# Kernel tuning notes

Measured on AMD Instinct MI355X. Metric: run time of the kernel, lower is better.

The kernel has to match this reference:

```python
import jax, jax.numpy as jnp
import numpy as np
from jax import lax
jax.config.update('jax_enable_x64', True)

SR = 44100
BLOCK = 512
N_MELS = 80
N_ALLPASS = 256
N_HARM = 512
N_NOISE = 256
HID = 256
B = 16
NF = 400
T = NF * BLOCK
N_OUT = N_ALLPASS + N_HARM + N_NOISE


def upsample(sig, factor):
    # torch: interpolate(cat(sig, sig[-1:]), size=n*factor+1, mode='linear', align_corners=True)[:-1]
    b, n, c = sig.shape
    ext = jnp.concatenate([sig, sig[:, -1:]], axis=1)  # (b, n+1, c)
    w = (jnp.arange(factor, dtype=jnp.float32) / factor)[None, None, :, None]
    up = ext[:, :-1, None, :] * (1.0 - w) + ext[:, 1:, None, :] * w
    return up.reshape(b, n * factor, c)


def hann_periodic(n):
    return 0.5 - 0.5 * jnp.cos(2.0 * np.pi * jnp.arange(n, dtype=jnp.float32) / n)


def freq_impulse_response(mag, hann_window, half_width=None):
    # mag: (b, nf, m) complex -> ir: (b, nf, 2*(m-1)) in causal (rolled) form
    ir = jnp.fft.irfft(mag).astype(jnp.float32)
    n = ir.shape[-1]
    if hann_window:
        if half_width is None:
            w = jnp.roll(hann_periodic(n), n // 2)
            ir = jnp.roll(ir * w, n // 2, axis=-1)
        else:
            # dynamic hann window with per-frame half width (b, nf, 1)
            w = jnp.arange(-(n // 2), (n + 1) // 2, dtype=jnp.float32) / half_width
            w = jnp.where(w > 1.0, 0.0, w)
            w = (1.0 + jnp.cos(np.pi * w)) * 0.5
            ir = jnp.roll(ir, n // 2, axis=-1) * w
    else:
        ir = jnp.roll(ir, n // 2, axis=-1)
    return ir


def fft_convolve(audio, ir):
    b, t = audio.shape
    nf, ir_size = ir.shape[1], ir.shape[2]
    hop = t // nf
    frame = 2 * hop
    fft_size = frame + ir_size - 1
    chunks = jnp.pad(audio, ((0, 0), (hop, hop))).reshape(b, nf + 2, hop)
    frames = jnp.concatenate([chunks[:, :-1], chunks[:, 1:]], axis=-1)  # (b, nf+1, frame)
    bart = 1.0 - jnp.abs(2.0 * jnp.arange(frame, dtype=jnp.float32) / frame - 1.0)
    frames = frames * bart
    ir_ext = jnp.concatenate([ir, ir[:, -1:]], axis=1)  # repeat last IR frame
    out_f = jnp.fft.irfft(jnp.fft.rfft(frames, fft_size) * jnp.fft.rfft(ir_ext, fft_size), fft_size).astype(jnp.float32)
    n_out = nf + 1
    length = (n_out - 1) * hop + fft_size
    idx = (jnp.arange(n_out)[:, None] * hop + jnp.arange(fft_size)[None, :]).reshape(-1)
    out = jnp.zeros((b, length), jnp.float32).at[:, idx].add(out_f.reshape(b, -1))
    return out[:, hop:t + hop]


def conv1d_same(x, w, bias):
    y = lax.conv_general_dilated(x, w, (1,), [(1, 1)], dimension_numbers=('NCH', 'OIH', 'NCH'))
    return y + bias[None, :, None]


def mel2ctrl(mel, phase, conv1_w, conv1_b, gn_g, gn_b, conv2_w, conv2_b, phase_w, phase_b, ln_g, ln_b, out_w, out_b):
    h = conv1d_same(mel.transpose(0, 2, 1), conv1_w, conv1_b)  # (b, 256, nf)
    b, c, l = h.shape
    g = h.reshape(b, 4, c // 4, l)  # GroupNorm(4, 256)
    mu = g.mean((2, 3), keepdims=True)
    var = g.var((2, 3), keepdims=True)
    h = ((g - mu) / jnp.sqrt(var + 1e-5)).reshape(b, c, l)
    h = h * gn_g[None, :, None] + gn_b[None, :, None]
    h = jnp.where(h >= 0, h, 0.01 * h)  # LeakyReLU
    h = conv1d_same(h, conv2_w, conv2_b).transpose(0, 2, 1)  # (b, nf, 256)
    pe = jnp.concatenate([jnp.sin(phase), jnp.cos(phase)], axis=-1) @ phase_w.T + phase_b
    h = h + pe
    mu = h.mean(-1, keepdims=True)
    var = h.var(-1, keepdims=True)
    h = (h - mu) / jnp.sqrt(var + 1e-5) * ln_g + ln_b
    out = h @ out_w.T + out_b
    gd = out[..., :N_ALLPASS]
    hm = out[..., N_ALLPASS:N_ALLPASS + N_HARM]
    nm = out[..., N_ALLPASS + N_HARM:]
    return gd, hm, nm


def setup_inputs():
    key = jax.random.key(0)
    ks = jax.random.split(key, 8)
    s = 0.02
    return {
        'mel_frames': jax.random.normal(ks[0], (B, NF, N_MELS), jnp.float32),
        'f0_frames': jax.random.uniform(ks[1], (B, NF, 1), jnp.float32) * 400.0 + 100.0,
        'initial_phase': jnp.zeros((B, 1, 1), jnp.float32),
        'uniform_noise': jax.random.uniform(ks[2], (B, T), jnp.float32),
        'conv1_w': jax.random.normal(ks[3], (HID, N_MELS, 3), jnp.float32) * s,
        'conv1_b': jnp.zeros((HID,), jnp.float32),
        'gn_g': jnp.ones((HID,), jnp.float32),
        'gn_b': jnp.zeros((HID,), jnp.float32),
        'conv2_w': jax.random.normal(ks[4], (HID, HID, 3), jnp.float32) * s,
        'conv2_b': jnp.zeros((HID,), jnp.float32),
        'phase_w': jax.random.normal(ks[5], (HID, 2), jnp.float32) * s,
        'phase_b': jnp.zeros((HID,), jnp.float32),
        'ln_g': jnp.ones((HID,), jnp.float32),
        'ln_b': jnp.zeros((HID,), jnp.float32),
        'out_w': jax.random.normal(ks[6], (N_OUT, HID), jnp.float32) * s,
        'out_b': jnp.zeros((N_OUT,), jnp.float32),
    }


def reference(mel_frames, f0_frames, initial_phase, uniform_noise, conv1_w, conv1_b, gn_g, gn_b, conv2_w, conv2_b, phase_w, phase_b, ln_g, ln_b, out_w, out_b):
    f0 = upsample(f0_frames, BLOCK)  # (B, T, 1)
    # double-precision wrapped phase accumulation
    x = jnp.cumsum(f0.astype(jnp.float64) / SR, axis=1) + initial_phase.astype(jnp.float64) / (2.0 * np.pi)
    x = (x - jnp.round(x)).astype(jnp.float32)
    phase_frames = 2.0 * np.pi * x[:, ::BLOCK, :]  # (B, NF, 1)
    gd_raw, hm_raw, nm_raw = mel2ctrl(mel_frames, phase_frames, conv1_w, conv1_b, gn_g, gn_b, conv2_w, conv2_b, phase_w, phase_b, ln_g, ln_b, out_w, out_b)
    group_delay = np.pi * jnp.tanh(gd_raw)
    src_param = jnp.exp(hm_raw)
    noise_param = jnp.exp(nm_raw) / 128.0
    combtooth = jnp.sinc(SR * x / (f0 + 0.001))[..., 0]  # (B, T)
    allpass = jnp.exp(1j * jnp.cumsum(group_delay, axis=-1).astype(jnp.complex64))
    harmonic = fft_convolve(combtooth, freq_impulse_response(allpass, hann_window=False))
    half_width = 1.5 * SR / (f0_frames + 0.001)  # (B, NF, 1)
    harmonic = fft_convolve(harmonic, freq_impulse_response(src_param.astype(jnp.complex64), True, half_width))
    noise = uniform_noise * 2.0 - 1.0
    noise = fft_convolve(noise, freq_impulse_response(noise_param.astype(jnp.complex64), True, None))
    signal = harmonic + noise
    return signal, phase_frames, harmonic, noise
```

## Files before the change

kernel.cpp:

```cpp
#include <hip/hip_runtime.h>
#include <math.h>

#define BATCH 16
#define NF_ 400
#define TLEN 204800
#define NMELS 80
#define HID 256
#define SRD 44100.0

static constexpr size_t S_   = 1638400;
static constexpr size_t FRSZ = (size_t)6416 * 1028;
static constexpr size_t OFF_A    = 0;
static constexpr size_t OFF_JN   = FRSZ;
static constexpr size_t OFF_SSP  = 2 * FRSZ;
static constexpr size_t OFF_IR1  = OFF_SSP + 2 * S_;
static constexpr size_t OFF_IR3  = OFF_IR1 + 3264000;
static constexpr size_t OFF_FSUM = OFF_IR3 + 3264000;
static constexpr size_t OFF_PREF = OFF_FSUM + 12800;
static constexpr size_t OFF_GN   = OFF_PREF + 12800;

__device__ __forceinline__ float cs8_f0_at(const float* f0f, int b, int n, int k) {
    float a = f0f[b * NF_ + n];
    float c = f0f[b * NF_ + min(n + 1, NF_ - 1)];
    float w = (float)k * (1.0f / 512.0f);
    return __fadd_rn(__fmul_rn(a, 1.0f - w), __fmul_rn(c, w));
}

__global__ void cs8_fsum(const float* __restrict__ f0f, double* __restrict__ fsum) {
    int gid = blockIdx.x * blockDim.x + threadIdx.x;
    if (gid >= BATCH * NF_) return;
    int b = gid / NF_, n = gid % NF_;
    double s = 0.0;
    for (int k = 0; k < 512; ++k) s += (double)cs8_f0_at(f0f, b, n, k) / SRD;
    fsum[gid] = s;
}

__global__ void cs8_prefix(const double* __restrict__ fsum, double* __restrict__ pref) {
    int b = threadIdx.x;
    if (b >= BATCH) return;
    double run = 0.0;
    for (int n = 0; n < NF_; ++n) { pref[b * NF_ + n] = run; run += fsum[b * NF_ + n]; }
}

__global__ __launch_bounds__(512) void cs8_phase(const float* __restrict__ f0f,
        const float* __restrict__ ip, const double* __restrict__ pref,
        float* __restrict__ frA, float* __restrict__ phase_out) {
    __shared__ double sc[512];
    int b = blockIdx.x / NF_, n = blockIdx.x % NF_;
    int k = threadIdx.x;
    float f0 = cs8_f0_at(f0f, b, n, k);
    sc[k] = (double)f0 / SRD;
    __syncthreads();
    for (int off = 1; off < 512; off <<= 1) {
        double v = (k >= off) ? sc[k - off] : 0.0;
        __syncthreads();
        sc[k] += v;
        __syncthreads();
    }
    double xd = pref[b * NF_ + n] + sc[k] + (double)ip[b] / (2.0 * M_PI);
    xd -= rint(xd);
    float xf = (float)xd;
    double zd = 44100.0 * (double)xf / ((double)f0 + 0.001);
    double pz = M_PI * zd;
    float cv = (zd == 0.0) ? 1.0f : (float)(sin(pz) / pz);
    float wb = (float)k * (1.0f / 512.0f);
    size_t row = (size_t)(b * 401 + n) * 1028;
    frA[row + 512 + k]  = cv * (1.0f - wb);
    frA[row + 1028 + k] = cv * wb;
    if (k == 0) phase_out[b * NF_ + n] = (float)(2.0 * M_PI * (double)xf);
}

__global__ __launch_bounds__(256) void cs8_conv1x3(const float* __restrict__ mel,
        const float* __restrict__ w1, const float* __restrict__ b1, float* __restrict__ h1) {
    __shared__ float m3[3][NMELS];
    int b = blockIdx.x / NF_, l = blockIdx.x % NF_;
    int tid = threadIdx.x;
    for (int i = tid; i < 3 * NMELS; i += 256) {
        int tap = i / NMELS, ic = i % NMELS;
        int li = l + tap - 1;
        m3[tap][ic] = (li >= 0 && li < NF_) ? mel[((size_t)b * NF_ + li) * NMELS + ic] : 0.0f;
    }
    __syncthreads();
    int oc = tid;
    double acc = (double)b1[oc];
    const float* wp = w1 + (size_t)oc * NMELS * 3;
    for (int ic = 0; ic < NMELS; ++ic)
        acc += (double)m3[0][ic] * (double)wp[ic * 3]
             + (double)m3[1][ic] * (double)wp[ic * 3 + 1]
             + (double)m3[2][ic] * (double)wp[ic * 3 + 2];
    h1[((size_t)b * NF_ + l) * HID + oc] = (float)acc;
}

__global__ __launch_bounds__(256) void cs8_gnstats(const float* __restrict__ h1, float* __restrict__ gn) {
    __shared__ double rs[256], rq[256];
    int b = blockIdx.x >> 2, g = blockIdx.x & 3;
    int tid = threadIdx.x;
    double s = 0.0, q = 0.0;
    for (int i = tid; i < 64 * NF_; i += 256) {
        int l = i >> 6, c = g * 64 + (i & 63);
        float v = h1[((size_t)b * NF_ + l) * HID + c];
        s += v; q += (double)v * v;
    }
    rs[tid] = s; rq[tid] = q;
    __syncthreads();
    for (int off = 128; off > 0; off >>= 1) {
        if (tid < off) { rs[tid] += rs[tid + off]; rq[tid] += rq[tid + off]; }
        __syncthreads();
    }
    if (tid == 0) {
        double mu = rs[0] / (64.0 * NF_);
        double var = rq[0] / (64.0 * NF_) - mu * mu;
        gn[blockIdx.x * 2] = (float)mu;
        gn[blockIdx.x * 2 + 1] = (float)(1.0 / sqrt(var + 1e-5));
    }
}

__global__ __launch_bounds__(256) void cs8_conv2ln(const float* __restrict__ h1,
        const float* __restrict__ gn, const float* __restrict__ gng, const float* __restrict__ gnb,
        const float* __restrict__ w2, const float* __restrict__ b2,
        const float* __restrict__ pw, const float* __restrict__ pb,
        const float* __restrict__ lng, const float* __restrict__ lnb,
        const float* __restrict__ phase, float* __restrict__ h2) {
    __shared__ float cols[10][HID];
    __shared__ double rsum[256], rsq[256];
    int b = blockIdx.x / 50, l0 = (blockIdx.x % 50) * 8;
    int tid = threadIdx.x;
    for (int i = tid; i < 10 * HID; i += 256) {
        int lc = i >> 8, c = i & 255;
        int l = l0 + lc - 1;
        float v = 0.0f;
        if (l >= 0 && l < NF_) {
            float hv = h1[((size_t)b * NF_ + l) * HID + c];
            int g = c >> 6;
            double vv = ((double)hv - (double)gn[(b * 4 + g) * 2]) * (double)gn[(b * 4 + g) * 2 + 1]
                        * (double)gng[c] + (double)gnb[c];
            v = (float)(vv >= 0.0 ? vv : 0.01 * vv);
        }
        cols[lc][c] = v;
    }
    __syncthreads();
    int oc = tid;
    double acc[8];
    #pragma unroll
    for (int lt = 0; lt < 8; ++lt) acc[lt] = (double)b2[oc];
    const float* wp = w2 + (size_t)oc * HID * 3;
    for (int ic = 0; ic < HID; ++ic) {
        double w0 = (double)wp[ic * 3], w1v = (double)wp[ic * 3 + 1], w2v = (double)wp[ic * 3 + 2];
        float cc[10];
        #pragma unroll
        for (int j = 0; j < 10; ++j) cc[j] = cols[j][ic];
        #pragma unroll
        for (int lt = 0; lt < 8; ++lt)
            acc[lt] += (double)cc[lt] * w0 + (double)cc[lt + 1] * w1v + (double)cc[lt + 2] * w2v;
    }
    for (int lt = 0; lt < 8; ++lt) {
        int l = l0 + lt;
        double ph = (double)phase[b * NF_ + l];
        double sp, cp; sincos(ph, &sp, &cp);
        double v = acc[lt] + sp * (double)pw[oc * 2] + cp * (double)pw[oc * 2 + 1] + (double)pb[oc];
        rsum[tid] = v; rsq[tid] = v * v;
        __syncthreads();
        for (int off = 128; off > 0; off >>= 1) {
            if (tid < off) { rsum[tid] += rsum[tid + off]; rsq[tid] += rsq[tid + off]; }
            __syncthreads();
        }
        double mu = rsum[0] * (1.0 / 256.0);
        double var = rsq[0] * (1.0 / 256.0) - mu * mu;
        double rstd = 1.0 / sqrt(var + 1e-5);
        __syncthreads();
        h2[((size_t)b * NF_ + l) * HID + oc] = (float)((v - mu) * rstd * (double)lng[oc] + (double)lnb[oc]);
    }
}

__global__ __launch_bounds__(256) void cs8_proj(const float* __restrict__ h2,
        const float* __restrict__ ow, const float* __restrict__ ob,
        float* __restrict__ phi, float* __restrict__ srcspec, float* __restrict__ nspec) {
    __shared__ float hrow[8][HID];
    __shared__ double ssc[256];
    int b = blockIdx.x / 50, l0 = (blockIdx.x % 50) * 8;
    int tid = threadIdx.x;
    for (int i = tid; i < 8 * HID; i += 256) {
        int lc = i >> 8, c = i & 255;
        hrow[lc][c] = h2[((size_t)b * NF_ + l0 + lc) * HID + c];
    }
    __syncthreads();
    double a0[8], a1[8], a2[8], a3[8];
    #pragma unroll
    for (int lt = 0; lt < 8; ++lt) {
        a0[lt] = (double)ob[tid];       a1[lt] = (double)ob[256 + tid];
        a2[lt] = (double)ob[512 + tid]; a3[lt] = (double)ob[768 + tid];
    }
    const float* w0p = ow + (size_t)tid * HID;
    const float* w1p = ow + (size_t)(256 + tid) * HID;
    const float* w2p = ow + (size_t)(512 + tid) * HID;
    const float* w3p = ow + (size_t)(768 + tid) * HID;
    for (int ic = 0; ic < HID; ++ic) {
        double w0 = (double)w0p[ic], w1v = (double)w1p[ic], w2v = (double)w2p[ic], w3v = (double)w3p[ic];
        #pragma unroll
        for (int lt = 0; lt < 8; ++lt) {
            double h = (double)hrow[lt][ic];
            a0[lt] += h * w0; a1[lt] += h * w1v; a2[lt] += h * w2v; a3[lt] += h * w3v;
        }
    }
    for (int lt = 0; lt < 8; ++lt) {
        size_t bl = (size_t)b * NF_ + (l0 + lt);
        double gdv = M_PI * tanh(a0[lt]);
        ssc[tid] = gdv;
        __syncthreads();
        for (int off = 1; off < 256; off <<= 1) {
            double v = (tid >= off) ? ssc[tid - off] : 0.0;
            __syncthreads();
            ssc[tid] += v;
            __syncthreads();
        }
        phi[bl * 256 + tid] = (float)ssc[tid];
        __syncthreads();
        srcspec[bl * 512 + tid] = (float)exp(a1[lt]);
        srcspec[bl * 512 + 256 + tid] = (float)exp(a2[lt]);
        nspec[bl * 256 + tid] = (float)(exp(a3[lt]) * (1.0 / 128.0));
    }
}

__global__ __launch_bounds__(256) void cs8_ir_allpass(const float* __restrict__ phi, float* __restrict__ ir1) {
    __shared__ float cph[256], sph[256];
    size_t bl = blockIdx.x;
    int tid = threadIdx.x;
    {
        float ph = phi[bl * 256 + tid];
        cph[tid] = 2.0f * cosf(ph); sph[tid] = 2.0f * sinf(ph);
    }
    __syncthreads();
    for (int t = tid; t < 510; t += 256) {
        double ang = 2.0 * M_PI * (double)t / 510.0;
        double srd_, crd; sincos(ang, &srd_, &crd);
        double sj, cj;    sincos(16.0 * ang, &sj, &cj);
        float crf = (float)crd, srf = (float)srd_;
        double cD = crd, sD = srd_;
        float acc = 0.5f * (cph[0] + ((t & 1) ? -cph[255] : cph[255]));
        for (int k0 = 1; k0 <= 254; k0 += 16) {
            float c = (float)cD, s = (float)sD;
            int ke = min(k0 + 16, 255);
            for (int k = k0; k < ke; ++k) {
                acc += cph[k] * c - sph[k] * s;
                float cn = c * crf - s * srf;
                float sn = s * crf + c * srf;
                c = cn; s = sn;
            }
            double nc = cD * cj - sD * sj;
            double ns = sD * cj + cD * sj;
            cD = nc; sD = ns;
        }
        int j = t + 255; if (j >= 510) j -= 510;
        ir1[bl * 510 + j] = acc * (1.0f / 510.0f);
    }
}

__device__ __forceinline__ float cs8_hw_win(int j, float hw) {
    float wv = (float)(j - 511) / hw;
    if (wv > 1.0f) wv = 0.0f;
    return (1.0f + cosf((float)M_PI * wv)) * 0.5f;
}

__global__ __launch_bounds__(256) void cs8_ir_src(const float* __restrict__ srcspec,
        const float* __restrict__ f0f, float* __restrict__ ir2) {
    __shared__ float sp[512];
    size_t bl = blockIdx.x;
    int b = blockIdx.x / NF_, l = blockIdx.x % NF_;
    int tid = threadIdx.x;
    sp[tid] = 2.0f * srcspec[bl * 512 + tid];
    sp[tid + 256] = 2.0f * srcspec[bl * 512 + 256 + tid];
    __syncthreads();
    float hw = 66150.0f / (f0f[b * NF_ + l] + 0.001f);
    for (int t = tid; t < 512; t += 256) {
        double ang = 2.0 * M_PI * (double)t / 1022.0;
        double srd_, crd; sincos(ang, &srd_, &crd);
        double sj, cj;    sincos(16.0 * ang, &sj, &cj);
        float crf = (float)crd, srf = (float)srd_;
        double cD = crd, sD = srd_;
        float acc = 0.5f * (sp[0] + ((t & 1) ? -sp[511] : sp[511]));
        for (int k0 = 1; k0 <= 510; k0 += 16) {
            float c = (float)cD, s = (float)sD;
            int ke = min(k0 + 16, 511);
            for (int k = k0; k < ke; ++k) {
                acc += sp[k] * c;
                float cn = c * crf - s * srf;
                float sn = s * crf + c * srf;
                c = cn; s = sn;
            }
            double nc = cD * cj - sD * sj;
            double ns = sD * cj + cD * sj;
            cD = nc; sD = ns;
        }
        float raw = acc * (1.0f / 1022.0f);
        {
            int j = t + 511; if (j >= 1022) j -= 1022;
            ir2[bl * 1022 + j] = raw * cs8_hw_win(j, hw);
        }
        if (t >= 1 && t <= 510) {
            int j = 511 - t;
            ir2[bl * 1022 + j] = raw * cs8_hw_win(j, hw);
        }
    }
}

__global__ __launch_bounds__(256) void cs8_ir_noise(const float* __restrict__ nspec, float* __restrict__ ir3) {
    __shared__ float sp[256];
    size_t bl = blockIdx.x;
    int t = threadIdx.x;
    sp[t] = 2.0f * nspec[bl * 256 + t];
    __syncthreads();
    double ang = 2.0 * M_PI * (double)t / 510.0;
    double srd_, crd; sincos(ang, &srd_, &crd);
    double sj, cj;    sincos(16.0 * ang, &sj, &cj);
    float crf = (float)crd, srf = (float)srd_;
    double cD = crd, sD = srd_;
    float acc = 0.5f * (sp[0] + ((t & 1) ? -sp[255] : sp[255]));
    for (int k0 = 1; k0 <= 254; k0 += 16) {
        float c = (float)cD, s = (float)sD;
        int ke = min(k0 + 16, 255);
        for (int k = k0; k < ke; ++k) {
            acc += sp[k] * c;
            float cn = c * crf - s * srf;
            float sn = s * crf + c * srf;
            c = cn; s = sn;
        }
        double nc = cD * cj - sD * sj;
        double ns = sD * cj + cD * sj;
        cD = nc; sD = ns;
    }
    float raw = acc * (1.0f / 510.0f);
    {
        int j = t + 255; if (j >= 510) j -= 510;
        float win = 0.5f - 0.5f * cosf((float)(2.0 * M_PI) * (float)j / 510.0f);
        ir3[bl * 510 + j] = raw * win;
    }
    if (t >= 1 && t <= 254) {
        int j = 255 - t;
        float win = 0.5f - 0.5f * cosf((float)(2.0 * M_PI) * (float)j / 510.0f);
        ir3[bl * 510 + j] = raw * win;
    }
}

__global__ __launch_bounds__(256) void cs8_stagef(const float* __restrict__ audio,
        float* __restrict__ frw, float scale, float shift) {
    int bm = blockIdx.x;
    int b = bm / 401, m = bm % 401;
    int tid = threadIdx.x;
    for (int kk = tid; kk < 1028; kk += 256) {
        float v = 0.0f;
        if (kk < 1024) {
            int idx = (m << 9) + kk - 512;
            if (idx >= 0 && idx < TLEN) {
                float a = audio[(size_t)b * TLEN + idx] * scale + shift;
                float bart = 1.0f - fabsf((float)kk * (1.0f / 512.0f) - 1.0f);
                v = a * bart;
            }
        }
        frw[(size_t)bm * 1028 + kk] = v;
    }
}

__device__ __forceinline__ int cs8_swz(int B) { return B ^ ((B >> 3) & 7); }

__device__ __forceinline__ void cs8_fma8(const float4 F, const float4 A,
        const float4 B, const float4 C, float acc[8]) {
    const float w[12] = {A.x,A.y,A.z,A.w,B.x,B.y,B.z,B.w,C.x,C.y,C.z,C.w};
    #pragma unroll
    for (int a = 0; a < 8; ++a)
        acc[a] += F.x * w[8 - a] + F.y * w[9 - a] + F.z * w[10 - a] + F.w * w[11 - a];
}

template<int IRS, int NFRM, int MOFF, int FOUT>
__global__ __launch_bounds__(256) void cs8_conv(const float* __restrict__ frw,
        const float* __restrict__ ir, float* __restrict__ out) {
    constexpr int PAD = 515;
    constexpr int R = IRS - 1 + PAD;
    constexpr int W = (R + 526) & ~3;
    __shared__ __align__(16) float sir[NFRM][W];
    int b = blockIdx.x / 100, q = blockIdx.x % 100;
    int t0 = q * 2048;
    int m_lo = (t0 >> 9) + MOFF;
    int tid = threadIdx.x;

    for (int i = tid; i < NFRM * W; i += 256) {
        int fi = i / W, x = i - fi * W;
        int j = R - x;
        int m = m_lo + fi;
        float v = 0.0f;
        if (j >= 0 && j < IRS && m >= 0 && m <= 400)
            v = ir[((size_t)b * NF_ + min(m, 399)) * IRS + j];
        int p = (cs8_swz(x >> 2) << 2) | (x & 3);
        sir[fi][p] = v;
    }
    __syncthreads();

    int tb = t0 + tid * 8;
    int wt0 = tid & ~63;
    float acc[8] = {0, 0, 0, 0, 0, 0, 0, 0};
    #pragma unroll
    for (int fi = 0; fi < NFRM; ++fi) {
        int m = m_lo + fi;
        if (m < 0 || m > 400) continue;
        int d0w = t0 + wt0 * 8 + 512 - (m << 9);
        int klo = max(0, d0w - (IRS - 1));
        int khi = min(1023, d0w + 511);
        if (klo > khi) continue;
        int kcs = __builtin_amdgcn_readfirstlane(klo & ~3);
        int nch = ((__builtin_amdgcn_readfirstlane(khi) - kcs) >> 2) + 1;
        int d0 = t0 + tid * 8 + 512 - (m << 9);
        int Bb = (R - d0 + kcs - 8) >> 2;
        const float4* row4 = (const float4*)&sir[fi][0];
        const float4* fp4 = (const float4*)(frw + (size_t)(b * 401 + m) * 1028 + kcs);
        float4 r0 = row4[cs8_swz(Bb)];
        float4 r1 = row4[cs8_swz(Bb + 1)];
        float4 r2;
        int c = 0;
        for (; c + 3 <= nch; c += 3) {
            float4 F0 = fp4[c];
            r2 = row4[cs8_swz(Bb + c + 2)];
            cs8_fma8(F0, r0, r1, r2, acc);
            float4 F1 = fp4[c + 1];
            r0 = row4[cs8_swz(Bb + c + 3)];
            cs8_fma8(F1, r1, r2, r0, acc);
            float4 F2 = fp4[c + 2];
            r1 = row4[cs8_swz(Bb + c + 4)];
            cs8_fma8(F2, r2, r0, r1, acc);
        }
        for (; c < nch; ++c) {
            float4 F = fp4[c];
            r2 = row4[cs8_swz(Bb + c + 2)];
            cs8_fma8(F, r0, r1, r2, acc);
            r0 = r1; r1 = r2;
        }
    }
    if (FOUT == 0) {
        float* o = out + (size_t)b * TLEN + tb;
        *(float4*)o = make_float4(acc[0], acc[1], acc[2], acc[3]);
        *(float4*)(o + 4) = make_float4(acc[4], acc[5], acc[6], acc[7]);
    } else {
        int km = tb & 511;
        int m1 = tb >> 9;
        float* r1p = out + (size_t)(b * 401 + m1) * 1028;
        float bw[8];
        #pragma unroll
        for (int j2 = 0; j2 < 8; ++j2) bw[j2] = (float)(km + j2) * (1.0f / 512.0f);
        *(float4*)(r1p + 512 + km) = make_float4(acc[0] * (1.f - bw[0]), acc[1] * (1.f - bw[1]),
                                                 acc[2] * (1.f - bw[2]), acc[3] * (1.f - bw[3]));
        *(float4*)(r1p + 512 + km + 4) = make_float4(acc[4] * (1.f - bw[4]), acc[5] * (1.f - bw[5]),
                                                     acc[6] * (1.f - bw[6]), acc[7] * (1.f - bw[7]));
        float* r2p = r1p + 1028;
        *(float4*)(r2p + km) = make_float4(acc[0] * bw[0], acc[1] * bw[1], acc[2] * bw[2], acc[3] * bw[3]);
        *(float4*)(r2p + km + 4) = make_float4(acc[4] * bw[4], acc[5] * bw[5], acc[6] * bw[6], acc[7] * bw[7]);
    }
}

__global__ void cs8_add(const float* __restrict__ a, const float* __restrict__ b,
                        float* __restrict__ o, int n4) {
    int i = blockIdx.x * blockDim.x + threadIdx.x;
    if (i < n4) {
        float4 x = ((const float4*)a)[i];
        float4 y = ((const float4*)b)[i];
        ((float4*)o)[i] = make_float4(x.x + y.x, x.y + y.y, x.z + y.z, x.w + y.w);
    }
}

extern "C" void kernel_launch(void* const* d_in, const int* in_sizes, int n_in,
                              void* d_out, int out_size, void* d_ws, size_t ws_size,
                              hipStream_t stream) {
    const float* mel   = (const float*)d_in[0];
    const float* f0f   = (const float*)d_in[1];
    const float* ip    = (const float*)d_in[2];
    const float* unoi  = (const float*)d_in[3];
    const float* w1    = (const float*)d_in[4];
    const float* b1    = (const float*)d_in[5];
    const float* gng   = (const float*)d_in[6];
    const float* gnb   = (const float*)d_in[7];
    const float* w2    = (const float*)d_in[8];
    const float* b2    = (const float*)d_in[9];
    const float* pw    = (const float*)d_in[10];
    const float* pb    = (const float*)d_in[11];
    const float* lng   = (const float*)d_in[12];
    const float* lnb   = (const float*)d_in[13];
    const float* ow    = (const float*)d_in[14];
    const float* ob    = (const float*)d_in[15];
    float* out = (float*)d_out;
    float* ws  = (float*)d_ws;

    float*  frA  = ws + OFF_A;
    float*  frJ  = ws + OFF_JN;
    float*  h1   = ws + OFF_JN;
    float*  h2   = ws + OFF_JN + S_;
    float*  phi  = ws + OFF_JN + 2 * S_;
    float*  nsp  = ws + OFF_JN + 3 * S_;
    float*  ssp  = ws + OFF_SSP;
    float*  ir1  = ws + OFF_IR1;
    float*  ir3  = ws + OFF_IR3;
    float*  ir2  = ws + OFF_A;
    double* fsum = (double*)(ws + OFF_FSUM);
    double* pref = (double*)(ws + OFF_PREF);
    float*  gn   = ws + OFF_GN;

    float* out_sig   = out;
    float* out_phase = out + (size_t)BATCH * TLEN;
    float* out_harm  = out_phase + BATCH * NF_;
    float* out_noise = out_harm + (size_t)BATCH * TLEN;

    hipMemsetAsync(frA, 0, FRSZ * sizeof(float), stream);
    cs8_fsum<<<25, 256, 0, stream>>>(f0f, fsum);
    cs8_prefix<<<1, 16, 0, stream>>>(fsum, pref);
    cs8_phase<<<BATCH * NF_, 512, 0, stream>>>(f0f, ip, pref, frA, out_phase);
    cs8_conv1x3<<<BATCH * NF_, 256, 0, stream>>>(mel, w1, b1, h1);
    cs8_gnstats<<<64, 256, 0, stream>>>(h1, gn);
    cs8_conv2ln<<<BATCH * 50, 256, 0, stream>>>(h1, gn, gng, gnb, w2, b2, pw, pb, lng, lnb, out_phase, h2);
    cs8_proj<<<BATCH * 50, 256, 0, stream>>>(h2, ow, ob, phi, ssp, nsp);
    cs8_ir_allpass<<<BATCH * NF_, 256, 0, stream>>>(phi, ir1);
    cs8_ir_noise<<<BATCH * NF_, 256, 0, stream>>>(nsp, ir3);
    cs8_stagef<<<BATCH * 401, 256, 0, stream>>>(unoi, frJ, 2.0f, -1.0f);
    cs8_conv<510, 6, -1, 0><<<BATCH * 100, 256, 0, stream>>>(frJ, ir3, out_noise);
    hipMemsetAsync(frJ, 0, FRSZ * sizeof(float), stream);
    cs8_conv<510, 6, -1, 1><<<BATCH * 100, 256, 0, stream>>>(frA, ir1, frJ);
    cs8_ir_src<<<BATCH * NF_, 256, 0, stream>>>(ssp, f0f, ir2);
    cs8_conv<1022, 7, -2, 0><<<BATCH * 100, 256, 0, stream>>>(frJ, ir2, out_harm);
    cs8_add<<<(BATCH * TLEN / 4 + 255) / 256, 256, 0, stream>>>(out_harm, out_noise, out_sig, BATCH * TLEN / 4);
}
```

Baseline: 2.819 ms.

## Stage frames in LDS and halve output tile for long-IR convolution

```diff
diff --git a/kernel.cpp b/kernel.cpp
--- a/kernel.cpp
+++ b/kernel.cpp
@@ -19,36 +19,36 @@
 static constexpr size_t OFF_PREF = OFF_FSUM + 12800;
 static constexpr size_t OFF_GN   = OFF_PREF + 12800;
 
-__device__ __forceinline__ float cs8_f0_at(const float* f0f, int b, int n, int k) {
+__device__ __forceinline__ float cs9_f0_at(const float* f0f, int b, int n, int k) {
     float a = f0f[b * NF_ + n];
     float c = f0f[b * NF_ + min(n + 1, NF_ - 1)];
     float w = (float)k * (1.0f / 512.0f);
     return __fadd_rn(__fmul_rn(a, 1.0f - w), __fmul_rn(c, w));
 }
 
-__global__ void cs8_fsum(const float* __restrict__ f0f, double* __restrict__ fsum) {
+__global__ void cs9_fsum(const float* __restrict__ f0f, double* __restrict__ fsum) {
     int gid = blockIdx.x * blockDim.x + threadIdx.x;
     if (gid >= BATCH * NF_) return;
     int b = gid / NF_, n = gid % NF_;
     double s = 0.0;
-    for (int k = 0; k < 512; ++k) s += (double)cs8_f0_at(f0f, b, n, k) / SRD;
+    for (int k = 0; k < 512; ++k) s += (double)cs9_f0_at(f0f, b, n, k) / SRD;
     fsum[gid] = s;
 }
 
-__global__ void cs8_prefix(const double* __restrict__ fsum, double* __restrict__ pref) {
+__global__ void cs9_prefix(const double* __restrict__ fsum, double* __restrict__ pref) {
     int b = threadIdx.x;
     if (b >= BATCH) return;
     double run = 0.0;
     for (int n = 0; n < NF_; ++n) { pref[b * NF_ + n] = run; run += fsum[b * NF_ + n]; }
 }
 
-__global__ __launch_bounds__(512) void cs8_phase(const float* __restrict__ f0f,
+__global__ __launch_bounds__(512) void cs9_phase(const float* __restrict__ f0f,
         const float* __restrict__ ip, const double* __restrict__ pref,
         float* __restrict__ frA, float* __restrict__ phase_out) {
     __shared__ double sc[512];
     int b = blockIdx.x / NF_, n = blockIdx.x % NF_;
     int k = threadIdx.x;
-    float f0 = cs8_f0_at(f0f, b, n, k);
+    float f0 = cs9_f0_at(f0f, b, n, k);
     sc[k] = (double)f0 / SRD;
     __syncthreads();
     for (int off = 1; off < 512; off <<= 1) {
@@ -70,7 +70,7 @@
     if (k == 0) phase_out[b * NF_ + n] = (float)(2.0 * M_PI * (double)xf);
 }
 
-__global__ __launch_bounds__(256) void cs8_conv1x3(const float* __restrict__ mel,
+__global__ __launch_bounds__(256) void cs9_conv1x3(const float* __restrict__ mel,
         const float* __restrict__ w1, const float* __restrict__ b1, float* __restrict__ h1) {
     __shared__ float m3[3][NMELS];
     int b = blockIdx.x / NF_, l = blockIdx.x % NF_;
@@ -91,7 +91,7 @@
     h1[((size_t)b * NF_ + l) * HID + oc] = (float)acc;
 }
 
-__global__ __launch_bounds__(256) void cs8_gnstats(const float* __restrict__ h1, float* __restrict__ gn) {
+__global__ __launch_bounds__(256) void cs9_gnstats(const float* __restrict__ h1, float* __restrict__ gn) {
     __shared__ double rs[256], rq[256];
     int b = blockIdx.x >> 2, g = blockIdx.x & 3;
     int tid = threadIdx.x;
@@ -115,7 +115,7 @@
     }
 }
 
-__global__ __launch_bounds__(256) void cs8_conv2ln(const float* __restrict__ h1,
+__global__ __launch_bounds__(256) void cs9_conv2ln(const float* __restrict__ h1,
         const float* __restrict__ gn, const float* __restrict__ gng, const float* __restrict__ gnb,
         const float* __restrict__ w2, const float* __restrict__ b2,
         const float* __restrict__ pw, const float* __restrict__ pb,
@@ -172,7 +172,7 @@
     }
 }
 
-__global__ __launch_bounds__(256) void cs8_proj(const float* __restrict__ h2,
+__global__ __launch_bounds__(256) void cs9_proj(const float* __restrict__ h2,
         const float* __restrict__ ow, const float* __restrict__ ob,
         float* __restrict__ phi, float* __restrict__ srcspec, float* __restrict__ nspec) {
     __shared__ float hrow[8][HID];
@@ -221,7 +221,7 @@
     }
 }
 
-__global__ __launch_bounds__(256) void cs8_ir_allpass(const float* __restrict__ phi, float* __restrict__ ir1) {
+__global__ __launch_bounds__(256) void cs9_ir_allpass(const float* __restrict__ phi, float* __restrict__ ir1) {
     __shared__ float cph[256], sph[256];
     size_t bl = blockIdx.x;
     int tid = threadIdx.x;
@@ -255,13 +255,13 @@
     }
 }
 
-__device__ __forceinline__ float cs8_hw_win(int j, float hw) {
+__device__ __forceinline__ float cs9_hw_win(int j, float hw) {
     float wv = (float)(j - 511) / hw;
     if (wv > 1.0f) wv = 0.0f;
     return (1.0f + cosf((float)M_PI * wv)) * 0.5f;
 }
 
-__global__ __launch_bounds__(256) void cs8_ir_src(const float* __restrict__ srcspec,
+__global__ __launch_bounds__(256) void cs9_ir_src(const float* __restrict__ srcspec,
         const float* __restrict__ f0f, float* __restrict__ ir2) {
     __shared__ float sp[512];
     size_t bl = blockIdx.x;
@@ -294,16 +294,16 @@
         float raw = acc * (1.0f / 1022.0f);
         {
             int j = t + 511; if (j >= 1022) j -= 1022;
-            ir2[bl * 1022 + j] = raw * cs8_hw_win(j, hw);
+            ir2[bl * 1022 + j] = raw * cs9_hw_win(j, hw);
         }
         if (t >= 1 && t <= 510) {
             int j = 511 - t;
-            ir2[bl * 1022 + j] = raw * cs8_hw_win(j, hw);
-        }
-    }
-}
-
-__global__ __launch_bounds__(256) void cs8_ir_noise(const float* __restrict__ nspec, float* __restrict__ ir3) {
+            ir2[bl * 1022 + j] = raw * cs9_hw_win(j, hw);
+        }
+    }
+}
+
+__global__ __launch_bounds__(256) void cs9_ir_noise(const float* __restrict__ nspec, float* __restrict__ ir3) {
     __shared__ float sp[256];
     size_t bl = blockIdx.x;
     int t = threadIdx.x;
@@ -341,7 +341,7 @@
     }
 }
 
-__global__ __launch_bounds__(256) void cs8_stagef(const float* __restrict__ audio,
+__global__ __launch_bounds__(256) void cs9_stagef(const float* __restrict__ audio,
         float* __restrict__ frw, float scale, float shift) {
     int bm = blockIdx.x;
     int b = bm / 401, m = bm % 401;
@@ -360,25 +360,18 @@
     }
 }
 
-__device__ __forceinline__ int cs8_swz(int B) { return B ^ ((B >> 3) & 7); }
-
-__device__ __forceinline__ void cs8_fma8(const float4 F, const float4 A,
-        const float4 B, const float4 C, float acc[8]) {
-    const float w[12] = {A.x,A.y,A.z,A.w,B.x,B.y,B.z,B.w,C.x,C.y,C.z,C.w};
-    #pragma unroll
-    for (int a = 0; a < 8; ++a)
-        acc[a] += F.x * w[8 - a] + F.y * w[9 - a] + F.z * w[10 - a] + F.w * w[11 - a];
-}
-
-template<int IRS, int NFRM, int MOFF, int FOUT>
-__global__ __launch_bounds__(256) void cs8_conv(const float* __restrict__ frw,
+__device__ __forceinline__ int cs9_swz(int B) { return B ^ ((B >> 3) & 7); }
+
+template<int IRS, int NFRM, int MOFF, int OUTS, int FOUT>
+__global__ __launch_bounds__(256) void cs9_conv(const float* __restrict__ frw,
         const float* __restrict__ ir, float* __restrict__ out) {
-    constexpr int PAD = 515;
-    constexpr int R = IRS - 1 + PAD;
-    constexpr int W = (R + 526) & ~3;
+    constexpr int TILE = 256 * OUTS;
+    constexpr int R = IRS + (OUTS == 8 ? 514 : 266);
+    constexpr int W = (R + (OUTS == 8 ? 515 : 259) + 3) & ~3;
     __shared__ __align__(16) float sir[NFRM][W];
-    int b = blockIdx.x / 100, q = blockIdx.x % 100;
-    int t0 = q * 2048;
+    __shared__ __align__(16) float sfr[NFRM][1028];
+    int b = blockIdx.x / (TLEN / TILE), q = blockIdx.x % (TLEN / TILE);
+    int t0 = q * TILE;
     int m_lo = (t0 >> 9) + MOFF;
     int tid = threadIdx.x;
 
@@ -389,72 +382,147 @@
         float v = 0.0f;
         if (j >= 0 && j < IRS && m >= 0 && m <= 400)
             v = ir[((size_t)b * NF_ + min(m, 399)) * IRS + j];
-        int p = (cs8_swz(x >> 2) << 2) | (x & 3);
+        int p = (OUTS == 8) ? ((cs9_swz(x >> 2) << 2) | (x & 3)) : x;
         sir[fi][p] = v;
     }
-    __syncthreads();
-
-    int tb = t0 + tid * 8;
+    for (int i = tid; i < NFRM * 257; i += 256) {
+        int fi = i / 257, x4 = i - fi * 257;
+        int m = m_lo + fi;
+        float4 v = make_float4(0.f, 0.f, 0.f, 0.f);
+        if (m >= 0 && m <= 400)
+            v = ((const float4*)(frw + (size_t)(b * 401 + m) * 1028))[x4];
+        ((float4*)&sfr[fi][0])[x4] = v;
+    }
+    __syncthreads();
+
+    int tb = t0 + tid * OUTS;
     int wt0 = tid & ~63;
-    float acc[8] = {0, 0, 0, 0, 0, 0, 0, 0};
+    float acc[OUTS];
+    #pragma unroll
+    for (int a = 0; a < OUTS; ++a) acc[a] = 0.0f;
+
     #pragma unroll
     for (int fi = 0; fi < NFRM; ++fi) {
         int m = m_lo + fi;
         if (m < 0 || m > 400) continue;
-        int d0w = t0 + wt0 * 8 + 512 - (m << 9);
+        int d0w = __builtin_amdgcn_readfirstlane(t0 + wt0 * OUTS + 512 - (m << 9));
         int klo = max(0, d0w - (IRS - 1));
-        int khi = min(1023, d0w + 511);
+        int khi = min(1023, d0w + 64 * OUTS - 1);
         if (klo > khi) continue;
-        int kcs = __builtin_amdgcn_readfirstlane(klo & ~3);
-        int nch = ((__builtin_amdgcn_readfirstlane(khi) - kcs) >> 2) + 1;
-        int d0 = t0 + tid * 8 + 512 - (m << 9);
-        int Bb = (R - d0 + kcs - 8) >> 2;
+        int kcs = klo & ~3;
+        int nch = ((khi - kcs) >> 2) + 1;
+        int d0 = t0 + tid * OUTS + 512 - (m << 9);
         const float4* row4 = (const float4*)&sir[fi][0];
-        const float4* fp4 = (const float4*)(frw + (size_t)(b * 401 + m) * 1028 + kcs);
-        float4 r0 = row4[cs8_swz(Bb)];
-        float4 r1 = row4[cs8_swz(Bb + 1)];
-        float4 r2;
-        int c = 0;
-        for (; c + 3 <= nch; c += 3) {
-            float4 F0 = fp4[c];
-            r2 = row4[cs8_swz(Bb + c + 2)];
-            cs8_fma8(F0, r0, r1, r2, acc);
-            float4 F1 = fp4[c + 1];
-            r0 = row4[cs8_swz(Bb + c + 3)];
-            cs8_fma8(F1, r1, r2, r0, acc);
-            float4 F2 = fp4[c + 2];
-            r1 = row4[cs8_swz(Bb + c + 4)];
-            cs8_fma8(F2, r2, r0, r1, acc);
-        }
-        for (; c < nch; ++c) {
-            float4 F = fp4[c];
-            r2 = row4[cs8_swz(Bb + c + 2)];
-            cs8_fma8(F, r0, r1, r2, acc);
-            r0 = r1; r1 = r2;
-        }
-    }
+        const float4* fp4 = (const float4*)&sfr[fi][0] + (kcs >> 2);
+
+        if (OUTS == 4) {
+            int Bb = (R - d0 + kcs - 4) >> 2;
+            float4 A = row4[Bb];
+            int c = 0;
+            for (; c + 2 <= nch; c += 2) {
+                float4 Bv = row4[Bb + c + 1];
+                float4 F0 = fp4[c];
+                acc[0] += F0.x * Bv.x + F0.y * Bv.y + F0.z * Bv.z + F0.w * Bv.w;
+                acc[1] += F0.x * A.w  + F0.y * Bv.x + F0.z * Bv.y + F0.w * Bv.z;
+                acc[2] += F0.x * A.z  + F0.y * A.w  + F0.z * Bv.x + F0.w * Bv.y;
+                acc[3] += F0.x * A.y  + F0.y * A.z  + F0.z * A.w  + F0.w * Bv.x;
+                float4 A2 = row4[Bb + c + 2];
+                float4 F1 = fp4[c + 1];
+                acc[0] += F1.x * A2.x + F1.y * A2.y + F1.z * A2.z + F1.w * A2.w;
+                acc[1] += F1.x * Bv.w + F1.y * A2.x + F1.z * A2.y + F1.w * A2.z;
+                acc[2] += F1.x * Bv.z + F1.y * Bv.w + F1.z * A2.x + F1.w * A2.y;
+                acc[3] += F1.x * Bv.y + F1.y * Bv.z + F1.z * Bv.w + F1.w * A2.x;
+                A = A2;
+            }
+            for (; c < nch; ++c) {
+                float4 Bv = row4[Bb + c + 1];
+                float4 F0 = fp4[c];
+                acc[0] += F0.x * Bv.x + F0.y * Bv.y + F0.z * Bv.z + F0.w * Bv.w;
+                acc[1] += F0.x * A.w  + F0.y * Bv.x + F0.z * Bv.y + F0.w * Bv.z;
+                acc[2] += F0.x * A.z  + F0.y * A.w  + F0.z * Bv.x + F0.w * Bv.y;
+                acc[3] += F0.x * A.y  + F0.y * A.z  + F0.z * A.w  + F0.w * Bv.x;
+                A = Bv;
+            }
+        } else {
+            int Bb = (R - d0 + kcs - 8) >> 2;
+            float4 A = row4[cs9_swz(Bb)];
+            float4 Bv = row4[cs9_swz(Bb + 1)];
+            float4 C;
+            int c = 0;
+            for (; c + 3 <= nch; c += 3) {
+                float4 F0 = fp4[c];
+                C = row4[cs9_swz(Bb + c + 2)];
+                acc[0] += F0.x*C.x + F0.y*C.y + F0.z*C.z + F0.w*C.w;
+                acc[1] += F0.x*Bv.w + F0.y*C.x + F0.z*C.y + F0.w*C.z;
+                acc[2] += F0.x*Bv.z + F0.y*Bv.w + F0.z*C.x + F0.w*C.y;
+                acc[3] += F0.x*Bv.y + F0.y*Bv.z + F0.z*Bv.w + F0.w*C.x;
+                acc[4] += F0.x*Bv.x + F0.y*Bv.y + F0.z*Bv.z + F0.w*Bv.w;
+                acc[5] += F0.x*A.w + F0.y*Bv.x + F0.z*Bv.y + F0.w*Bv.z;
+                acc[6] += F0.x*A.z + F0.y*A.w + F0.z*Bv.x + F0.w*Bv.y;
+                acc[7] += F0.x*A.y + F0.y*A.z + F0.z*A.w + F0.w*Bv.x;
+                float4 F1 = fp4[c + 1];
+                A = row4[cs9_swz(Bb + c + 3)];
+                acc[0] += F1.x*A.x + F1.y*A.y + F1.z*A.z + F1.w*A.w;
+                acc[1] += F1.x*C.w + F1.y*A.x + F1.z*A.y + F1.w*A.z;
+                acc[2] += F1.x*C.z + F1.y*C.w + F1.z*A.x + F1.w*A.y;
+                acc[3] += F1.x*C.y + F1.y*C.z + F1.z*C.w + F1.w*A.x;
+                acc[4] += F1.x*C.x + F1.y*C.y + F1.z*C.z + F1.w*C.w;
+                acc[5] += F1.x*Bv.w + F1.y*C.x + F1.z*C.y + F1.w*C.z;
+                acc[6] += F1.x*Bv.z + F1.y*Bv.w + F1.z*C.x + F1.w*C.y;
+                acc[7] += F1.x*Bv.y + F1.y*Bv.z + F1.z*Bv.w + F1.w*C.x;
+                float4 F2 = fp4[c + 2];
+                Bv = row4[cs9_swz(Bb + c + 4)];
+                acc[0] += F2.x*Bv.x + F2.y*Bv.y + F2.z*Bv.z + F2.w*Bv.w;
+                acc[1] += F2.x*A.w + F2.y*Bv.x + F2.z*Bv.y + F2.w*Bv.z;
+                acc[2] += F2.x*A.z + F2.y*A.w + F2.z*Bv.x + F2.w*Bv.y;
+                acc[3] += F2.x*A.y + F2.y*A.z + F2.z*A.w + F2.w*Bv.x;
+                acc[4] += F2.x*A.x + F2.y*A.y + F2.z*A.z + F2.w*A.w;
+                acc[5] += F2.x*C.w + F2.y*A.x + F2.z*A.y + F2.w*A.z;
+                acc[6] += F2.x*C.z + F2.y*C.w + F2.z*A.x + F2.w*A.y;
+                acc[7] += F2.x*C.y + F2.y*C.z + F2.z*C.w + F2.w*A.x;
+            }
+            for (; c < nch; ++c) {
+                float4 F0 = fp4[c];
+                C = row4[cs9_swz(Bb + c + 2)];
+                acc[0] += F0.x*C.x + F0.y*C.y + F0.z*C.z + F0.w*C.w;
+                acc[1] += F0.x*Bv.w + F0.y*C.x + F0.z*C.y + F0.w*C.z;
+                acc[2] += F0.x*Bv.z + F0.y*Bv.w + F0.z*C.x + F0.w*C.y;
+                acc[3] += F0.x*Bv.y + F0.y*Bv.z + F0.z*Bv.w + F0.w*C.x;
+                acc[4] += F0.x*Bv.x + F0.y*Bv.y + F0.z*Bv.z + F0.w*Bv.w;
+                acc[5] += F0.x*A.w + F0.y*Bv.x + F0.z*Bv.y + F0.w*Bv.z;
+                acc[6] += F0.x*A.z + F0.y*A.w + F0.z*Bv.x + F0.w*Bv.y;
+                acc[7] += F0.x*A.y + F0.y*A.z + F0.z*A.w + F0.w*Bv.x;
+                A = Bv; Bv = C;
+            }
+        }
+    }
+
     if (FOUT == 0) {
         float* o = out + (size_t)b * TLEN + tb;
-        *(float4*)o = make_float4(acc[0], acc[1], acc[2], acc[3]);
-        *(float4*)(o + 4) = make_float4(acc[4], acc[5], acc[6], acc[7]);
+        #pragma unroll
+        for (int a4 = 0; a4 < OUTS; a4 += 4)
+            *(float4*)(o + a4) = make_float4(acc[a4], acc[a4+1], acc[a4+2], acc[a4+3]);
     } else {
         int km = tb & 511;
         int m1 = tb >> 9;
         float* r1p = out + (size_t)(b * 401 + m1) * 1028;
-        float bw[8];
+        float* r2p = r1p + 1028;
+        float bw[OUTS];
         #pragma unroll
-        for (int j2 = 0; j2 < 8; ++j2) bw[j2] = (float)(km + j2) * (1.0f / 512.0f);
-        *(float4*)(r1p + 512 + km) = make_float4(acc[0] * (1.f - bw[0]), acc[1] * (1.f - bw[1]),
-                                                 acc[2] * (1.f - bw[2]), acc[3] * (1.f - bw[3]));
-        *(float4*)(r1p + 512 + km + 4) = make_float4(acc[4] * (1.f - bw[4]), acc[5] * (1.f - bw[5]),
-                                                     acc[6] * (1.f - bw[6]), acc[7] * (1.f - bw[7]));
-        float* r2p = r1p + 1028;
-        *(float4*)(r2p + km) = make_float4(acc[0] * bw[0], acc[1] * bw[1], acc[2] * bw[2], acc[3] * bw[3]);
-        *(float4*)(r2p + km + 4) = make_float4(acc[4] * bw[4], acc[5] * bw[5], acc[6] * bw[6], acc[7] * bw[7]);
-    }
-}
-
-__global__ void cs8_add(const float* __restrict__ a, const float* __restrict__ b,
+        for (int j2 = 0; j2 < OUTS; ++j2) bw[j2] = (float)(km + j2) * (1.0f / 512.0f);
+        #pragma unroll
+        for (int a4 = 0; a4 < OUTS; a4 += 4) {
+            *(float4*)(r1p + 512 + km + a4) = make_float4(
+                acc[a4] * (1.f - bw[a4]), acc[a4+1] * (1.f - bw[a4+1]),
+                acc[a4+2] * (1.f - bw[a4+2]), acc[a4+3] * (1.f - bw[a4+3]));
+            *(float4*)(r2p + km + a4) = make_float4(
+                acc[a4] * bw[a4], acc[a4+1] * bw[a4+1],
+                acc[a4+2] * bw[a4+2], acc[a4+3] * bw[a4+3]);
+        }
+    }
+}
+
+__global__ void cs9_add(const float* __restrict__ a, const float* __restrict__ b,
                         float* __restrict__ o, int n4) {
     int i = blockIdx.x * blockDim.x + threadIdx.x;
     if (i < n4) {
@@ -506,20 +574,20 @@
     float* out_noise = out_harm + (size_t)BATCH * TLEN;
 
     hipMemsetAsync(frA, 0, FRSZ * sizeof(float), stream);
-    cs8_fsum<<<25, 256, 0, stream>>>(f0f, fsum);
-    cs8_prefix<<<1, 16, 0, stream>>>(fsum, pref);
-    cs8_phase<<<BATCH * NF_, 512, 0, stream>>>(f0f, ip, pref, frA, out_phase);
-    cs8_conv1x3<<<BATCH * NF_, 256, 0, stream>>>(mel, w1, b1, h1);
-    cs8_gnstats<<<64, 256, 0, stream>>>(h1, gn);
-    cs8_conv2ln<<<BATCH * 50, 256, 0, stream>>>(h1, gn, gng, gnb, w2, b2, pw, pb, lng, lnb, out_phase, h2);
-    cs8_proj<<<BATCH * 50, 256, 0, stream>>>(h2, ow, ob, phi, ssp, nsp);
-    cs8_ir_allpass<<<BATCH * NF_, 256, 0, stream>>>(phi, ir1);
-    cs8_ir_noise<<<BATCH * NF_, 256, 0, stream>>>(nsp, ir3);
-    cs8_stagef<<<BATCH * 401, 256, 0, stream>>>(unoi, frJ, 2.0f, -1.0f);
-    cs8_conv<510, 6, -1, 0><<<BATCH * 100, 256, 0, stream>>>(frJ, ir3, out_noise);
+    cs9_fsum<<<25, 256, 0, stream>>>(f0f, fsum);
+    cs9_prefix<<<1, 16, 0, stream>>>(fsum, pref);
+    cs9_phase<<<BATCH * NF_, 512, 0, stream>>>(f0f, ip, pref, frA, out_phase);
+    cs9_conv1x3<<<BATCH * NF_, 256, 0, stream>>>(mel, w1, b1, h1);
+    cs9_gnstats<<<64, 256, 0, stream>>>(h1, gn);
+    cs9_conv2ln<<<BATCH * 50, 256, 0, stream>>>(h1, gn, gng, gnb, w2, b2, pw, pb, lng, lnb, out_phase, h2);
+    cs9_proj<<<BATCH * 50, 256, 0, stream>>>(h2, ow, ob, phi, ssp, nsp);
+    cs9_ir_allpass<<<BATCH * NF_, 256, 0, stream>>>(phi, ir1);
+    cs9_ir_noise<<<BATCH * NF_, 256, 0, stream>>>(nsp, ir3);
+    cs9_stagef<<<BATCH * 401, 256, 0, stream>>>(unoi, frJ, 2.0f, -1.0f);
+    cs9_conv<510, 6, -1, 8, 0><<<BATCH * 100, 256, 0, stream>>>(frJ, ir3, out_noise);
     hipMemsetAsync(frJ, 0, FRSZ * sizeof(float), stream);
-    cs8_conv<510, 6, -1, 1><<<BATCH * 100, 256, 0, stream>>>(frA, ir1, frJ);
-    cs8_ir_src<<<BATCH * NF_, 256, 0, stream>>>(ssp, f0f, ir2);
-    cs8_conv<1022, 7, -2, 0><<<BATCH * 100, 256, 0, stream>>>(frJ, ir2, out_harm);
-    cs8_add<<<(BATCH * TLEN / 4 + 255) / 256, 256, 0, stream>>>(out_harm, out_noise, out_sig, BATCH * TLEN / 4);
-}
+    cs9_conv<510, 6, -1, 8, 1><<<BATCH * 100, 256, 0, stream>>>(frA, ir1, frJ);
+    cs9_ir_src<<<BATCH * NF_, 256, 0, stream>>>(ssp, f0f, ir2);
+    cs9_conv<1022, 5, -2, 4, 0><<<BATCH * 200, 256, 0, stream>>>(frJ, ir2, out_harm);
+    cs9_add<<<(BATCH * TLEN / 4 + 255) / 256, 256, 0, stream>>>(out_harm, out_noise, out_sig, BATCH * TLEN / 4);
+}
```

After: 2.714 ms. 3.7% less time.
